# Performance work log

Hardware: AMD Instinct MI355X
Metric: run time of the kernel (lower is better)

## Reference

```python
import jax, jax.numpy as jnp
import numpy as np

N_EMBD = 1024
N_HEAD = 16
HEAD_SIZE = N_EMBD // N_HEAD
SEQ_LEN = 2048


def setup_inputs() -> dict:
    key = jax.random.key(0)
    k_x, k_wa, k_ba, k_wp, k_bp = jax.random.split(key, 5)
    s = 0.02
    return {
        "x": jax.random.normal(k_x, (4, SEQ_LEN, N_EMBD), dtype=jnp.float32),
        "w_attn": jax.random.normal(k_wa, (N_EMBD, 3 * N_EMBD), dtype=jnp.float32) * s,
        "b_attn": jax.random.normal(k_ba, (3 * N_EMBD,), dtype=jnp.float32) * s,
        "w_proj": jax.random.normal(k_wp, (N_EMBD, N_EMBD), dtype=jnp.float32) * s,
        "b_proj": jax.random.normal(k_bp, (N_EMBD,), dtype=jnp.float32) * s,
    }


def reference(x, w_attn, b_attn, w_proj, b_proj):
    B, T, C = x.shape
    H, D = N_HEAD, HEAD_SIZE
    qkv = x @ w_attn + b_attn                      # [B,T,3C]
    q, k, v = jnp.split(qkv, 3, axis=-1)
    q = q.reshape(B, T, H, D).transpose(0, 2, 1, 3)  # [B,H,T,D]
    k = k.reshape(B, T, H, D).transpose(0, 2, 1, 3)
    v = v.reshape(B, T, H, D).transpose(0, 2, 1, 3)
    att = jnp.einsum('bhqd,bhkd->bhqk', q, k) / jnp.sqrt(jnp.float32(D))
    causal = jnp.tril(jnp.ones((T, T), dtype=bool))
    att = jnp.where(causal[None, None], att, jnp.float32(-jnp.inf))
    att = jax.nn.softmax(att, axis=-1)
    out = jnp.einsum('bhqk,bhkd->bhqd', att, v)    # [B,H,T,D]
    out = out.transpose(0, 2, 1, 3).reshape(B, T, C)
    return out @ w_proj + b_proj
```

## Files before the change

kernel.cpp:

```cpp
#include <hip/hip_runtime.h>

typedef short short8 __attribute__((ext_vector_type(8)));
typedef short short4v __attribute__((ext_vector_type(4)));
typedef float f32x4 __attribute__((ext_vector_type(4)));
typedef unsigned uint2v __attribute__((ext_vector_type(2)));

__device__ __forceinline__ float bf2f(short b) {
  unsigned u = ((unsigned)(unsigned short)b) << 16;
  return __builtin_bit_cast(float, u);
}
__device__ __forceinline__ short f2bf(float f) {
  unsigned u = __builtin_bit_cast(unsigned, f);
  u += 0x7fffu + ((u >> 16) & 1u);
  return (short)(u >> 16);
}
__device__ __forceinline__ unsigned cvt_pk_bf16(float lo, float hi) {
  unsigned r;
  asm("v_cvt_pk_bf16_f32 %0, %1, %2" : "=v"(r) : "v"(lo), "v"(hi));
  return r;
}

__device__ __forceinline__ void gload_lds16(const void* g, void* l) {
  __builtin_amdgcn_global_load_lds(
      (const __attribute__((address_space(1))) unsigned int*)g,
      (__attribute__((address_space(3))) unsigned int*)l, 16, 0, 0);
}

__device__ __forceinline__ short8 lds_frag(const short* tile, int row, int kc, int l4) {
  int chunk = (kc * 4 + l4) ^ (row & 7);
  return *(const short8*)&tile[row * 64 + chunk * 8];
}

__global__ __launch_bounds__(256) void k_convert_bf16(const float* __restrict__ in,
                                                      short* __restrict__ out, int n8) {
  int i = blockIdx.x * 256 + threadIdx.x;
  if (i >= n8) return;
  const float4* p = (const float4*)in;
  float4 a = p[2 * i], b = p[2 * i + 1];
  short8 o;
  o[0] = f2bf(a.x); o[1] = f2bf(a.y); o[2] = f2bf(a.z); o[3] = f2bf(a.w);
  o[4] = f2bf(b.x); o[5] = f2bf(b.y); o[6] = f2bf(b.z); o[7] = f2bf(b.w);
  ((short8*)out)[i] = o;
}

__global__ __launch_bounds__(256) void k_transpose_w(const float* __restrict__ w,
                                                     short* __restrict__ wT, int K, int N) {
  __shared__ float t[32][33];
  int nt = N >> 5;
  int rt = blockIdx.x / nt, ct = blockIdx.x % nt;
  int tx = threadIdx.x & 31, ty = threadIdx.x >> 5;
#pragma unroll
  for (int i = 0; i < 4; ++i) {
    int r = ty * 4 + i;
    t[r][tx] = w[(size_t)(rt * 32 + r) * N + ct * 32 + tx];
  }
  __syncthreads();
#pragma unroll
  for (int i = 0; i < 4; ++i) {
    int r = ty * 4 + i;
    wT[(size_t)(ct * 32 + r) * K + rt * 32 + tx] = f2bf(t[tx][r]);
  }
}

template <bool BF16OUT>
__global__ __launch_bounds__(512, 1) void k_gemm8p(const short* __restrict__ A,
                                                   const short* __restrict__ Bt,
                                                   const float* __restrict__ bias,
                                                   void* __restrict__ Cout,
                                                   short* __restrict__ vTout,
                                                   int M, int N, int K) {
  __shared__ __align__(16) short Ab[2][256 * 64];
  __shared__ __align__(16) short Bb[2][256 * 64];
  int nt = N >> 8;
  int nwg = gridDim.x;
  int bid = blockIdx.x;
  int swz = (bid & 7) * (nwg >> 3) + (bid >> 3);
  int mt = swz / nt, ct = swz % nt;
  int tid = threadIdx.x, w = tid >> 6, lane = tid & 63;
  int l15 = lane & 15, l4 = lane >> 4;
  int wm = w >> 2, wn = w & 3;
  const short* Abase = A + (size_t)mt * 256 * K;
  const short* Bbase = Bt + (size_t)ct * 256 * K;
  int NT = K >> 6;

  int srow = lane >> 3;
  int slc = (lane & 7) ^ srow;

  auto stage = [&](const short* gbase, short* dstTile, int kt, int half) {
#pragma unroll
    for (int i = 0; i < 2; ++i) {
      int rowg = half * 128 + i * 64 + w * 8;
      gload_lds16(gbase + (size_t)(rowg + srow) * K + kt * 64 + slc * 8,
                  dstTile + (size_t)rowg * 64);
    }
  };

  f32x4 acc[8][4];
#pragma unroll
  for (int m = 0; m < 8; ++m)
#pragma unroll
    for (int n = 0; n < 4; ++n) acc[m][n] = f32x4{0.f, 0.f, 0.f, 0.f};

  stage(Bbase, &Bb[0][0], 0, 0);
  stage(Bbase, &Bb[0][0], 0, 1);
  stage(Abase, &Ab[0][0], 0, 0);
  stage(Abase, &Ab[0][0], 0, 1);
  stage(Bbase, &Bb[1][0], 1, 0);
  stage(Bbase, &Bb[1][0], 1, 1);
  stage(Abase, &Ab[1][0], 1, 0);
  stage(Abase, &Ab[1][0], 1, 1);
  asm volatile("s_waitcnt vmcnt(8)" ::: "memory");
  __builtin_amdgcn_s_barrier();

  for (int t = 0; t < NT; ++t) {
    int b = t & 1;
    const short* At = &Ab[b][0];
    const short* Btl = &Bb[b][0];
    short* Aw = &Ab[b][0];
    short* Bw = &Bb[b][0];
    bool pre = (t + 2 < NT);

    short8 aflo[4][2], bflo[2][2], bfhi[2][2], afhi[4][2];
#pragma unroll
    for (int mq = 0; mq < 4; ++mq)
#pragma unroll
      for (int kc = 0; kc < 2; ++kc)
        aflo[mq][kc] = lds_frag(At, wm * 128 + mq * 16 + l15, kc, l4);
#pragma unroll
    for (int nq = 0; nq < 2; ++nq)
#pragma unroll
      for (int kc = 0; kc < 2; ++kc)
        bflo[nq][kc] = lds_frag(Btl, wn * 64 + nq * 16 + l15, kc, l4);
    __builtin_amdgcn_s_barrier();
    asm volatile("s_waitcnt lgkmcnt(0)" ::: "memory");
    __builtin_amdgcn_sched_barrier(0);
    __builtin_amdgcn_s_setprio(1);
#pragma unroll
    for (int mq = 0; mq < 4; ++mq)
#pragma unroll
      for (int nq = 0; nq < 2; ++nq)
#pragma unroll
        for (int kc = 0; kc < 2; ++kc)
          acc[mq][nq] = __builtin_amdgcn_mfma_f32_16x16x32_bf16(aflo[mq][kc], bflo[nq][kc], acc[mq][nq], 0, 0, 0);
    __builtin_amdgcn_s_setprio(0);
    __builtin_amdgcn_s_barrier();

#pragma unroll
    for (int nq = 0; nq < 2; ++nq)
#pragma unroll
      for (int kc = 0; kc < 2; ++kc)
        bfhi[nq][kc] = lds_frag(Btl, wn * 64 + 32 + nq * 16 + l15, kc, l4);
    __builtin_amdgcn_s_barrier();
    asm volatile("s_waitcnt lgkmcnt(0)" ::: "memory");
    __builtin_amdgcn_sched_barrier(0);
    __builtin_amdgcn_s_setprio(1);
#pragma unroll
    for (int mq = 0; mq < 4; ++mq)
#pragma unroll
      for (int nq = 0; nq < 2; ++nq)
#pragma unroll
        for (int kc = 0; kc < 2; ++kc)
          acc[mq][2 + nq] = __builtin_amdgcn_mfma_f32_16x16x32_bf16(aflo[mq][kc], bfhi[nq][kc], acc[mq][2 + nq], 0, 0, 0);
    __builtin_amdgcn_s_setprio(0);
    __builtin_amdgcn_s_barrier();

#pragma unroll
    for (int mq = 0; mq < 4; ++mq)
#pragma unroll
      for (int kc = 0; kc < 2; ++kc)
        afhi[mq][kc] = lds_frag(At, wm * 128 + 64 + mq * 16 + l15, kc, l4);
    if (pre) {
      stage(Bbase, Bw, t + 2, 0);
      stage(Bbase, Bw, t + 2, 1);
    }
    __builtin_amdgcn_s_barrier();
    asm volatile("s_waitcnt lgkmcnt(0)" ::: "memory");
    __builtin_amdgcn_sched_barrier(0);
    __builtin_amdgcn_s_setprio(1);
#pragma unroll
    for (int mq = 0; mq < 4; ++mq)
#pragma unroll
      for (int nq = 0; nq < 2; ++nq)
#pragma unroll
        for (int kc = 0; kc < 2; ++kc)
          acc[4 + mq][2 + nq] = __builtin_amdgcn_mfma_f32_16x16x32_bf16(afhi[mq][kc], bfhi[nq][kc], acc[4 + mq][2 + nq], 0, 0, 0);
    __builtin_amdgcn_s_setprio(0);
    __builtin_amdgcn_s_barrier();

    if (pre) {
      stage(Abase, Aw, t + 2, 0);
      stage(Abase, Aw, t + 2, 1);
    }
    __builtin_amdgcn_s_setprio(1);
#pragma unroll
    for (int mq = 0; mq < 4; ++mq)
#pragma unroll
      for (int nq = 0; nq < 2; ++nq)
#pragma unroll
        for (int kc = 0; kc < 2; ++kc)
          acc[4 + mq][nq] = __builtin_amdgcn_mfma_f32_16x16x32_bf16(afhi[mq][kc], bflo[nq][kc], acc[4 + mq][nq], 0, 0, 0);
    __builtin_amdgcn_s_setprio(0);
    if (pre) {
      asm volatile("s_waitcnt vmcnt(8)" ::: "memory");
    } else if (t + 1 < NT) {
      asm volatile("s_waitcnt vmcnt(0)" ::: "memory");
    }
    __builtin_amdgcn_s_barrier();
  }

#pragma unroll
  for (int m = 0; m < 8; ++m) {
#pragma unroll
    for (int n = 0; n < 4; ++n) {
      int row = mt * 256 + wm * 128 + m * 16 + l4 * 4;
      int col = ct * 256 + wn * 64 + n * 16 + l15;
      float bv = bias[col];
      if constexpr (BF16OUT) {
        short4v pk4;
#pragma unroll
        for (int j = 0; j < 4; ++j) pk4[j] = f2bf(acc[m][n][j] + bv);
        if (col >= 2048) {
          int hh = (col - 2048) >> 6, dd = (col - 2048) & 63;
          int batch2 = row >> 11, tok = row & 2047;
          *(short4v*)(vTout + (((size_t)(batch2 * 16 + hh) * 64 + dd) << 11) + tok) = pk4;
        } else {
#pragma unroll
          for (int j = 0; j < 4; ++j)
            ((short*)Cout)[(size_t)(row + j) * N + col] = pk4[j];
        }
      } else {
#pragma unroll
        for (int j = 0; j < 4; ++j)
          ((float*)Cout)[(size_t)(row + j) * N + col] = acc[m][n][j] + bv;
      }
    }
  }
}

template <bool BF16OUT>
__global__ __launch_bounds__(256) void k_gemm_bt(const short* __restrict__ A,
                                                 const short* __restrict__ Bt,
                                                 const float* __restrict__ bias,
                                                 void* __restrict__ Cout,
                                                 int M, int N, int K) {
  __shared__ __align__(16) short As[128 * 32];
  __shared__ __align__(16) short Bs[128 * 32];
  int nt = N >> 7;
  int mt = blockIdx.x / nt, ct = blockIdx.x % nt;
  int tid = threadIdx.x, w = tid >> 6, lane = tid & 63;
  int l15 = lane & 15, l4 = lane >> 4;
  int wr = (w >> 1) * 64, wc = (w & 1) * 64;
  const short* Abase = A + (size_t)mt * 128 * K;
  const short* Bbase = Bt + (size_t)ct * 128 * K;
  f32x4 acc[4][4];
#pragma unroll
  for (int m = 0; m < 4; ++m)
#pragma unroll
    for (int n = 0; n < 4; ++n) acc[m][n] = f32x4{0.f, 0.f, 0.f, 0.f};

  for (int kt = 0; kt < K; kt += 32) {
    __syncthreads();
#pragma unroll
    for (int i = 0; i < 2; ++i) {
      int idx = (w * 2 + i) * 64 + lane;
      gload_lds16(Abase + (size_t)(idx >> 2) * K + kt + (idx & 3) * 8, &As[(w * 2 + i) * 512]);
      gload_lds16(Bbase + (size_t)(idx >> 2) * K + kt + (idx & 3) * 8, &Bs[(w * 2 + i) * 512]);
    }
    __syncthreads();
    short8 af[4], bfr[4];
#pragma unroll
    for (int m = 0; m < 4; ++m) af[m] = *(const short8*)&As[(wr + m * 16 + l15) * 32 + l4 * 8];
#pragma unroll
    for (int n = 0; n < 4; ++n) bfr[n] = *(const short8*)&Bs[(wc + n * 16 + l15) * 32 + l4 * 8];
#pragma unroll
    for (int m = 0; m < 4; ++m)
#pragma unroll
      for (int n = 0; n < 4; ++n)
        acc[m][n] = __builtin_amdgcn_mfma_f32_16x16x32_bf16(af[m], bfr[n], acc[m][n], 0, 0, 0);
  }

#pragma unroll
  for (int m = 0; m < 4; ++m) {
#pragma unroll
    for (int n = 0; n < 4; ++n) {
      int row = mt * 128 + wr + m * 16 + l4 * 4;
      int col = ct * 128 + wc + n * 16 + l15;
      float bv = bias[col];
#pragma unroll
      for (int j = 0; j < 4; ++j) {
        float v = acc[m][n][j] + bv;
        if constexpr (BF16OUT)
          ((short*)Cout)[(size_t)(row + j) * N + col] = f2bf(v);
        else
          ((float*)Cout)[(size_t)(row + j) * N + col] = v;
      }
    }
  }
}

__global__ __launch_bounds__(256, 2) void k_attn(const short* __restrict__ qkv,
                                                 const short* __restrict__ vT,
                                                 short* __restrict__ out) {
  constexpr int T = 2048, C3 = 3072;
  __shared__ __align__(16) short Kl[2][64 * 72];
  __shared__ __align__(16) short P_lds[4][2][32 * 72];
  int i_ = blockIdx.x;
  int xcd = i_ & 7, m_ = i_ >> 3;
  int bh = xcd * 8 + (m_ & 7), bp = m_ >> 3;
  int batch = bh >> 4, h = bh & 15;
  int tid = threadIdx.x, w = tid >> 6, lane = tid & 63;
  int l15 = lane & 15, l4 = lane >> 4;

  int qt[2];
  qt[0] = 63 - (bp * 4 + w);
  qt[1] = bp * 4 + w;
  int lim[2] = {qt[0] >> 1, qt[1] >> 1};
  int ktb = (63 - bp * 4) >> 1;

  const short* kbase = qkv + (size_t)(batch * T) * C3 + 1024 + h * 64;
  const short* vbase = vT + (size_t)bh * 64 * T;

  int sr0 = tid >> 3, sr1 = 32 + (tid >> 3), sdc = (tid & 7) * 8;

  const float SCL = 0.18033688f;
  short8 qf[2][2][2];
#pragma unroll
  for (int t = 0; t < 2; ++t)
#pragma unroll
    for (int qc = 0; qc < 2; ++qc) {
      const short* qrow = qkv + (size_t)(batch * T + qt[t] * 32 + qc * 16 + l15) * C3 + h * 64;
#pragma unroll
      for (int kc = 0; kc < 2; ++kc) {
        short8 v = *(const short8*)(qrow + kc * 32 + l4 * 8);
#pragma unroll
        for (int i = 0; i < 8; ++i) v[i] = f2bf(bf2f(v[i]) * SCL);
        qf[t][qc][kc] = v;
      }
    }

  const f32x4 ZERO = f32x4{0.f, 0.f, 0.f, 0.f};
  short8 ONES;
#pragma unroll
  for (int i = 0; i < 8; ++i) ONES[i] = (short)0x3F80;

  f32x4 o_[2][2][4];
  f32x4 lacc[2][2];
#pragma unroll
  for (int t = 0; t < 2; ++t)
#pragma unroll
    for (int qc = 0; qc < 2; ++qc) {
      lacc[t][qc] = ZERO;
#pragma unroll
      for (int dt = 0; dt < 4; ++dt) o_[t][qc][dt] = ZERO;
    }

  {
    short8 a = *(const short8*)(kbase + (size_t)sr0 * C3 + sdc);
    short8 b = *(const short8*)(kbase + (size_t)sr1 * C3 + sdc);
    *(short8*)&Kl[0][sr0 * 72 + sdc] = a;
    *(short8*)&Kl[0][sr1 * 72 + sdc] = b;
  }
  __syncthreads();

  int cur = 0;
  for (int kt = 0; kt <= ktb; ++kt) {
    bool more = (kt < ktb);
    bool act0 = (kt <= lim[0]), act1 = (kt <= lim[1]);

    short8 pre0, pre1;
    if (more) {
      pre0 = *(const short8*)(kbase + (size_t)((kt + 1) * 64 + sr0) * C3 + sdc);
      pre1 = *(const short8*)(kbase + (size_t)((kt + 1) * 64 + sr1) * C3 + sdc);
    }

    const short* Kb = &Kl[cur][0];
    short8 kf[4][2];
#pragma unroll
    for (int kvt = 0; kvt < 4; ++kvt)
#pragma unroll
      for (int kc = 0; kc < 2; ++kc)
        kf[kvt][kc] = *(const short8*)(Kb + (kvt * 16 + l15) * 72 + kc * 32 + l4 * 8);

    short8 vf[4][2];
#pragma unroll
    for (int dt = 0; dt < 4; ++dt)
#pragma unroll
      for (int kc = 0; kc < 2; ++kc)
        vf[dt][kc] = *(const short8*)(vbase + (size_t)(dt * 16 + l15) * T + kt * 64 + kc * 32 + l4 * 8);

#pragma unroll
    for (int t = 0; t < 2; ++t) {
      bool act = (t == 0) ? act0 : act1;
      if (!act) continue;
      short* pb = &P_lds[w][t][0];

#pragma unroll
      for (int qc = 0; qc < 2; ++qc) {
        f32x4 s[4];
        __builtin_amdgcn_s_setprio(1);
#pragma unroll
        for (int kvt = 0; kvt < 4; ++kvt) {
          s[kvt] = __builtin_amdgcn_mfma_f32_16x16x32_bf16(kf[kvt][0], qf[t][qc][0], ZERO, 0, 0, 0);
          s[kvt] = __builtin_amdgcn_mfma_f32_16x16x32_bf16(kf[kvt][1], qf[t][qc][1], s[kvt], 0, 0, 0);
        }
        __builtin_amdgcn_s_setprio(0);

        if (kt == lim[t]) {
          int qg = qt[t] * 32 + qc * 16 + l15;
#pragma unroll
          for (int kvt = 0; kvt < 4; ++kvt)
#pragma unroll
            for (int j = 0; j < 4; ++j) {
              int kg = kt * 64 + kvt * 16 + l4 * 4 + j;
              if (kg > qg) s[kvt][j] = -1e30f;
            }
        }

#pragma unroll
        for (int kvt = 0; kvt < 4; ++kvt) {
          float p0 = exp2f(s[kvt][0]);
          float p1 = exp2f(s[kvt][1]);
          float p2 = exp2f(s[kvt][2]);
          float p3 = exp2f(s[kvt][3]);
          unsigned lo = cvt_pk_bf16(p0, p1);
          unsigned hi = cvt_pk_bf16(p2, p3);
          *(uint2v*)(pb + (qc * 16 + l15) * 72 + kvt * 16 + l4 * 4) = uint2v{lo, hi};
        }
      }
    }

    asm volatile("s_waitcnt lgkmcnt(0)" ::: "memory");

    __builtin_amdgcn_s_setprio(1);
#pragma unroll
    for (int t = 0; t < 2; ++t) {
      bool act = (t == 0) ? act0 : act1;
      if (!act) continue;
      const short* pb = &P_lds[w][t][0];
#pragma unroll
      for (int qc = 0; qc < 2; ++qc)
#pragma unroll
        for (int kc = 0; kc < 2; ++kc) {
          short8 pf = *(const short8*)(pb + (qc * 16 + l15) * 72 + kc * 32 + l4 * 8);
          lacc[t][qc] = __builtin_amdgcn_mfma_f32_16x16x32_bf16(ONES, pf, lacc[t][qc], 0, 0, 0);
#pragma unroll
          for (int dt = 0; dt < 4; ++dt)
            o_[t][qc][dt] = __builtin_amdgcn_mfma_f32_16x16x32_bf16(vf[dt][kc], pf, o_[t][qc][dt], 0, 0, 0);
        }
    }
    __builtin_amdgcn_s_setprio(0);

    if (more) {
      *(short8*)&Kl[cur ^ 1][sr0 * 72 + sdc] = pre0;
      *(short8*)&Kl[cur ^ 1][sr1 * 72 + sdc] = pre1;
    }
    __syncthreads();
    cur ^= 1;
  }

#pragma unroll
  for (int t = 0; t < 2; ++t) {
#pragma unroll
    for (int qc = 0; qc < 2; ++qc) {
      float inv = 1.f / lacc[t][qc][0];
      size_t rowb = (size_t)(batch * T + qt[t] * 32 + qc * 16 + l15) * 1024 + h * 64;
#pragma unroll
      for (int dt = 0; dt < 4; ++dt) {
        short4v pk4;
#pragma unroll
        for (int j = 0; j < 4; ++j) pk4[j] = f2bf(o_[t][qc][dt][j] * inv);
        *(short4v*)(out + rowb + dt * 16 + l4 * 4) = pk4;
      }
    }
  }
}

extern "C" void kernel_launch(void* const* d_in, const int* in_sizes, int n_in,
                              void* d_out, int out_size, void* d_ws, size_t ws_size,
                              hipStream_t stream) {
  const float* x      = (const float*)d_in[0];
  const float* w_attn = (const float*)d_in[1];
  const float* b_attn = (const float*)d_in[2];
  const float* w_proj = (const float*)d_in[3];
  const float* b_proj = (const float*)d_in[4];
  float* out = (float*)d_out;

  char* ws = (char*)d_ws;
  short* xb   = (short*)(ws);
  short* waT  = (short*)(ws + 16777216);
  short* wpT  = (short*)(ws + 23068672);
  short* qkv  = (short*)(ws + 25165824);
  short* vT   = (short*)(ws + 75497472);
  short* attn = xb;

  k_convert_bf16<<<4096, 256, 0, stream>>>(x, xb, 1048576);
  k_transpose_w<<<32 * 96, 256, 0, stream>>>(w_attn, waT, 1024, 3072);
  k_transpose_w<<<32 * 32, 256, 0, stream>>>(w_proj, wpT, 1024, 1024);
  k_gemm8p<true><<<384, 512, 0, stream>>>(xb, waT, b_attn, qkv, vT, 8192, 3072, 1024);
  k_attn<<<512, 256, 0, stream>>>(qkv, vT, attn);
  k_gemm_bt<false><<<64 * 8, 256, 0, stream>>>(attn, wpT, b_proj, out, 8192, 1024, 1024);
}
```

Before: 197.2 us.

## Shrink gemm8p N-tile to 128 and reuse it for output projection

Changes the pipelined 8-wave GEMM from a 256x256 tile to a 256x128 tile, halving B staging and accumulators, and doubles the QKV grid to 768 blocks. The simple k_gemm_bt kernel for the output projection is removed and replaced by the pipelined kernel with fp32 output on 256 blocks. The aim is better CU occupancy (more blocks than the 256 CUs) and a faster projection GEMM, at the cost of less reuse of A per block and more redundant A loads.

```diff
diff --git a/kernel.cpp b/kernel.cpp
--- a/kernel.cpp
+++ b/kernel.cpp
@@ -70,8 +70,8 @@
                                                    short* __restrict__ vTout,
                                                    int M, int N, int K) {
   __shared__ __align__(16) short Ab[2][256 * 64];
-  __shared__ __align__(16) short Bb[2][256 * 64];
-  int nt = N >> 8;
+  __shared__ __align__(16) short Bb[2][128 * 64];
+  int nt = N >> 7;
   int nwg = gridDim.x;
   int bid = blockIdx.x;
   int swz = (bid & 7) * (nwg >> 3) + (bid >> 3);
@@ -80,7 +80,7 @@
   int l15 = lane & 15, l4 = lane >> 4;
   int wm = w >> 2, wn = w & 3;
   const short* Abase = A + (size_t)mt * 256 * K;
-  const short* Bbase = Bt + (size_t)ct * 256 * K;
+  const short* Bbase = Bt + (size_t)ct * 128 * K;
   int NT = K >> 6;
 
   int srow = lane >> 3;
@@ -95,21 +95,19 @@
     }
   };
 
-  f32x4 acc[8][4];
+  f32x4 acc[8][2];
 #pragma unroll
   for (int m = 0; m < 8; ++m)
 #pragma unroll
-    for (int n = 0; n < 4; ++n) acc[m][n] = f32x4{0.f, 0.f, 0.f, 0.f};
+    for (int n = 0; n < 2; ++n) acc[m][n] = f32x4{0.f, 0.f, 0.f, 0.f};
 
   stage(Bbase, &Bb[0][0], 0, 0);
-  stage(Bbase, &Bb[0][0], 0, 1);
   stage(Abase, &Ab[0][0], 0, 0);
   stage(Abase, &Ab[0][0], 0, 1);
   stage(Bbase, &Bb[1][0], 1, 0);
-  stage(Bbase, &Bb[1][0], 1, 1);
   stage(Abase, &Ab[1][0], 1, 0);
   stage(Abase, &Ab[1][0], 1, 1);
-  asm volatile("s_waitcnt vmcnt(8)" ::: "memory");
+  asm volatile("s_waitcnt vmcnt(6)" ::: "memory");
   __builtin_amdgcn_s_barrier();
 
   for (int t = 0; t < NT; ++t) {
@@ -120,17 +118,16 @@
     short* Bw = &Bb[b][0];
     bool pre = (t + 2 < NT);
 
-    short8 aflo[4][2], bflo[2][2], bfhi[2][2], afhi[4][2];
+    short8 aflo[4][2], bflo[2], bfhi[2], afhi[4][2];
+
 #pragma unroll
     for (int mq = 0; mq < 4; ++mq)
 #pragma unroll
       for (int kc = 0; kc < 2; ++kc)
         aflo[mq][kc] = lds_frag(At, wm * 128 + mq * 16 + l15, kc, l4);
 #pragma unroll
-    for (int nq = 0; nq < 2; ++nq)
-#pragma unroll
-      for (int kc = 0; kc < 2; ++kc)
-        bflo[nq][kc] = lds_frag(Btl, wn * 64 + nq * 16 + l15, kc, l4);
+    for (int kc = 0; kc < 2; ++kc)
+      bflo[kc] = lds_frag(Btl, wn * 32 + l15, kc, l4);
     __builtin_amdgcn_s_barrier();
     asm volatile("s_waitcnt lgkmcnt(0)" ::: "memory");
     __builtin_amdgcn_sched_barrier(0);
@@ -138,18 +135,14 @@
 #pragma unroll
     for (int mq = 0; mq < 4; ++mq)
 #pragma unroll
-      for (int nq = 0; nq < 2; ++nq)
-#pragma unroll
-        for (int kc = 0; kc < 2; ++kc)
-          acc[mq][nq] = __builtin_amdgcn_mfma_f32_16x16x32_bf16(aflo[mq][kc], bflo[nq][kc], acc[mq][nq], 0, 0, 0);
+      for (int kc = 0; kc < 2; ++kc)
+        acc[mq][0] = __builtin_amdgcn_mfma_f32_16x16x32_bf16(aflo[mq][kc], bflo[kc], acc[mq][0], 0, 0, 0);
     __builtin_amdgcn_s_setprio(0);
     __builtin_amdgcn_s_barrier();
 
 #pragma unroll
-    for (int nq = 0; nq < 2; ++nq)
-#pragma unroll
-      for (int kc = 0; kc < 2; ++kc)
-        bfhi[nq][kc] = lds_frag(Btl, wn * 64 + 32 + nq * 16 + l15, kc, l4);
+    for (int kc = 0; kc < 2; ++kc)
+      bfhi[kc] = lds_frag(Btl, wn * 32 + 16 + l15, kc, l4);
     __builtin_amdgcn_s_barrier();
     asm volatile("s_waitcnt lgkmcnt(0)" ::: "memory");
     __builtin_amdgcn_sched_barrier(0);
@@ -157,10 +150,8 @@
 #pragma unroll
     for (int mq = 0; mq < 4; ++mq)
 #pragma unroll
-      for (int nq = 0; nq < 2; ++nq)
-#pragma unroll
-        for (int kc = 0; kc < 2; ++kc)
-          acc[mq][2 + nq] = __builtin_amdgcn_mfma_f32_16x16x32_bf16(aflo[mq][kc], bfhi[nq][kc], acc[mq][2 + nq], 0, 0, 0);
+      for (int kc = 0; kc < 2; ++kc)
+        acc[mq][1] = __builtin_amdgcn_mfma_f32_16x16x32_bf16(aflo[mq][kc], bfhi[kc], acc[mq][1], 0, 0, 0);
     __builtin_amdgcn_s_setprio(0);
     __builtin_amdgcn_s_barrier();
 
@@ -169,10 +160,7 @@
 #pragma unroll
       for (int kc = 0; kc < 2; ++kc)
         afhi[mq][kc] = lds_frag(At, wm * 128 + 64 + mq * 16 + l15, kc, l4);
-    if (pre) {
-      stage(Bbase, Bw, t + 2, 0);
-      stage(Bbase, Bw, t + 2, 1);
-    }
+    if (pre) stage(Bbase, Bw, t + 2, 0);
     __builtin_amdgcn_s_barrier();
     asm volatile("s_waitcnt lgkmcnt(0)" ::: "memory");
     __builtin_amdgcn_sched_barrier(0);
@@ -180,10 +168,8 @@
 #pragma unroll
     for (int mq = 0; mq < 4; ++mq)
 #pragma unroll
-      for (int nq = 0; nq < 2; ++nq)
-#pragma unroll
-        for (int kc = 0; kc < 2; ++kc)
-          acc[4 + mq][2 + nq] = __builtin_amdgcn_mfma_f32_16x16x32_bf16(afhi[mq][kc], bfhi[nq][kc], acc[4 + mq][2 + nq], 0, 0, 0);
+      for (int kc = 0; kc < 2; ++kc)
+        acc[4 + mq][1] = __builtin_amdgcn_mfma_f32_16x16x32_bf16(afhi[mq][kc], bfhi[kc], acc[4 + mq][1], 0, 0, 0);
     __builtin_amdgcn_s_setprio(0);
     __builtin_amdgcn_s_barrier();
 
@@ -195,13 +181,11 @@
 #pragma unroll
     for (int mq = 0; mq < 4; ++mq)
 #pragma unroll
-      for (int nq = 0; nq < 2; ++nq)
-#pragma unroll
-        for (int kc = 0; kc < 2; ++kc)
-          acc[4 + mq][nq] = __builtin_amdgcn_mfma_f32_16x16x32_bf16(afhi[mq][kc], bflo[nq][kc], acc[4 + mq][nq], 0, 0, 0);
+      for (int kc = 0; kc < 2; ++kc)
+        acc[4 + mq][0] = __builtin_amdgcn_mfma_f32_16x16x32_bf16(afhi[mq][kc], bflo[kc], acc[4 + mq][0], 0, 0, 0);
     __builtin_amdgcn_s_setprio(0);
     if (pre) {
-      asm volatile("s_waitcnt vmcnt(8)" ::: "memory");
+      asm volatile("s_waitcnt vmcnt(6)" ::: "memory");
     } else if (t + 1 < NT) {
       asm volatile("s_waitcnt vmcnt(0)" ::: "memory");
     }
@@ -211,9 +195,9 @@
 #pragma unroll
   for (int m = 0; m < 8; ++m) {
 #pragma unroll
-    for (int n = 0; n < 4; ++n) {
+    for (int n = 0; n < 2; ++n) {
       int row = mt * 256 + wm * 128 + m * 16 + l4 * 4;
-      int col = ct * 256 + wn * 64 + n * 16 + l15;
+      int col = ct * 128 + wn * 32 + n * 16 + l15;
       float bv = bias[col];
       if constexpr (BF16OUT) {
         short4v pk4;
@@ -232,67 +216,6 @@
 #pragma unroll
         for (int j = 0; j < 4; ++j)
           ((float*)Cout)[(size_t)(row + j) * N + col] = acc[m][n][j] + bv;
-      }
-    }
-  }
-}
-
-template <bool BF16OUT>
-__global__ __launch_bounds__(256) void k_gemm_bt(const short* __restrict__ A,
-                                                 const short* __restrict__ Bt,
-                                                 const float* __restrict__ bias,
-                                                 void* __restrict__ Cout,
-                                                 int M, int N, int K) {
-  __shared__ __align__(16) short As[128 * 32];
-  __shared__ __align__(16) short Bs[128 * 32];
-  int nt = N >> 7;
-  int mt = blockIdx.x / nt, ct = blockIdx.x % nt;
-  int tid = threadIdx.x, w = tid >> 6, lane = tid & 63;
-  int l15 = lane & 15, l4 = lane >> 4;
-  int wr = (w >> 1) * 64, wc = (w & 1) * 64;
-  const short* Abase = A + (size_t)mt * 128 * K;
-  const short* Bbase = Bt + (size_t)ct * 128 * K;
-  f32x4 acc[4][4];
-#pragma unroll
-  for (int m = 0; m < 4; ++m)
-#pragma unroll
-    for (int n = 0; n < 4; ++n) acc[m][n] = f32x4{0.f, 0.f, 0.f, 0.f};
-
-  for (int kt = 0; kt < K; kt += 32) {
-    __syncthreads();
-#pragma unroll
-    for (int i = 0; i < 2; ++i) {
-      int idx = (w * 2 + i) * 64 + lane;
-      gload_lds16(Abase + (size_t)(idx >> 2) * K + kt + (idx & 3) * 8, &As[(w * 2 + i) * 512]);
-      gload_lds16(Bbase + (size_t)(idx >> 2) * K + kt + (idx & 3) * 8, &Bs[(w * 2 + i) * 512]);
-    }
-    __syncthreads();
-    short8 af[4], bfr[4];
-#pragma unroll
-    for (int m = 0; m < 4; ++m) af[m] = *(const short8*)&As[(wr + m * 16 + l15) * 32 + l4 * 8];
-#pragma unroll
-    for (int n = 0; n < 4; ++n) bfr[n] = *(const short8*)&Bs[(wc + n * 16 + l15) * 32 + l4 * 8];
-#pragma unroll
-    for (int m = 0; m < 4; ++m)
-#pragma unroll
-      for (int n = 0; n < 4; ++n)
-        acc[m][n] = __builtin_amdgcn_mfma_f32_16x16x32_bf16(af[m], bfr[n], acc[m][n], 0, 0, 0);
-  }
-
-#pragma unroll
-  for (int m = 0; m < 4; ++m) {
-#pragma unroll
-    for (int n = 0; n < 4; ++n) {
-      int row = mt * 128 + wr + m * 16 + l4 * 4;
-      int col = ct * 128 + wc + n * 16 + l15;
-      float bv = bias[col];
-#pragma unroll
-      for (int j = 0; j < 4; ++j) {
-        float v = acc[m][n][j] + bv;
-        if constexpr (BF16OUT)
-          ((short*)Cout)[(size_t)(row + j) * N + col] = f2bf(v);
-        else
-          ((float*)Cout)[(size_t)(row + j) * N + col] = v;
       }
     }
   }
@@ -496,7 +419,7 @@
   k_convert_bf16<<<4096, 256, 0, stream>>>(x, xb, 1048576);
   k_transpose_w<<<32 * 96, 256, 0, stream>>>(w_attn, waT, 1024, 3072);
   k_transpose_w<<<32 * 32, 256, 0, stream>>>(w_proj, wpT, 1024, 1024);
-  k_gemm8p<true><<<384, 512, 0, stream>>>(xb, waT, b_attn, qkv, vT, 8192, 3072, 1024);
+  k_gemm8p<true><<<768, 512, 0, stream>>>(xb, waT, b_attn, qkv, vT, 8192, 3072, 1024);
   k_attn<<<512, 256, 0, stream>>>(qkv, vT, attn);
-  k_gemm_bt<false><<<64 * 8, 256, 0, stream>>>(attn, wpT, b_proj, out, 8192, 1024, 1024);
-}
+  k_gemm8p<false><<<256, 512, 0, stream>>>(attn, wpT, b_proj, out, nullptr, 8192, 1024, 1024);
+}
```

Result: no change. 198.3 us (+0.6%).
